# Optimization experiments

Measured on AMD Instinct MI355X. Metric: run time of the kernel, lower is better.

The kernel has to match this reference:

```python
import jax, jax.numpy as jnp
import numpy as np

N = 100000   # nodes
E = 1600000  # edges
D = 64       # feature dim (input = hidden = output)
G = 256      # graphs in batch
EPS = 1e-5   # BatchNorm eps


def setup_inputs() -> dict:
    key = jax.random.key(0)
    ks = jax.random.split(key, 16)
    inp = {
        "x": jax.random.normal(ks[0], (N, D), dtype=jnp.float32),
        "edge_index": jax.random.randint(ks[1], (2, E), 0, N, dtype=jnp.int64),
        "batch": jnp.sort(jax.random.randint(ks[2], (N,), 0, G, dtype=jnp.int64)),
    }
    # GCNConv weights (glorot-ish) + biases, and BatchNorm affine params, 3 layers
    for i in range(3):
        inp[f"W{i+1}"] = jax.random.normal(ks[3 + i], (D, D), dtype=jnp.float32) / np.sqrt(D)
        inp[f"b{i+1}"] = jnp.zeros((D,), dtype=jnp.float32)
        inp[f"g{i+1}"] = jnp.ones((D,), dtype=jnp.float32)   # BN gamma
        inp[f"be{i+1}"] = jnp.zeros((D,), dtype=jnp.float32)  # BN beta
    return inp


def _batchnorm(x, gamma, beta):
    # BatchNorm1d in training mode: batch stats over the node dim (biased var)
    mean = jnp.mean(x, axis=0)
    var = jnp.mean(jnp.square(x - mean), axis=0)
    return (x - mean) * jax.lax.rsqrt(var + EPS) * gamma + beta


def reference(x, edge_index, batch, W1, b1, g1, be1, W2, b2, g2, be2, W3, b3, g3, be3):
    src, dst = edge_index[0], edge_index[1]
    # GCN normalization with self-loops: norm_ij = deg_i^-1/2 * deg_j^-1/2 over A + I
    loop = jnp.arange(N, dtype=src.dtype)
    src2 = jnp.concatenate([src, loop])
    dst2 = jnp.concatenate([dst, loop])
    deg = jax.ops.segment_sum(jnp.ones_like(src2, dtype=x.dtype), dst2, num_segments=N)
    dinv = jax.lax.rsqrt(deg)  # deg >= 1 thanks to self loops
    norm = (dinv[src2] * dinv[dst2])[:, None]  # [E+N, 1]

    def gcn_conv(h, W, b):
        h = h @ W                                   # [N, D] small GEMM
        msg = h[src2] * norm                        # per-edge gather (memory bound)
        return jax.ops.segment_sum(msg, dst2, num_segments=N) + b

    params = [(W1, b1, g1, be1), (W2, b2, g2, be2), (W3, b3, g3, be3)]
    h = x
    for i, (W, b, g, be) in enumerate(params):
        h = gcn_conv(h, W, b)
        h = _batchnorm(h, g, be)
        if i < 2:
            h = jax.nn.relu(h)
            # dropout(p=0.2) is identity in deterministic/eval reference

    # global mean + max pool per graph
    ones = jnp.ones((N,), dtype=h.dtype)
    cnt = jax.ops.segment_sum(ones, batch, num_segments=G)            # [G]
    s = jax.ops.segment_sum(h, batch, num_segments=G)                 # [G, D]
    mean = s / jnp.maximum(cnt, 1.0)[:, None]
    mx = jax.ops.segment_max(h, batch, num_segments=G)
    mx = jnp.where(cnt[:, None] > 0, mx, 0.0)
    return mean + mx
```

## Files before the change

### kernel.cpp

```cpp
#include <hip/hip_runtime.h>
#include <hip/hip_bf16.h>
#include <math.h>

#define N_NODES 100000
#define N_EDGES 1600000
#define DIM 64
#define N_GRAPHS 256
#define BN_EPS 1e-5f
#define N_XCD 8
#define BUCKET ((N_NODES + N_XCD - 1) / N_XCD)
#define FILL_CHUNKS 128
#define FILL_ESIZE ((N_EDGES + FILL_CHUNKS - 1) / FILL_CHUNKS)
#define CSR_STRIDE 48
#define HIST_BLOCKS (FILL_CHUNKS * N_XCD)
#define GEMM0_BLOCKS 1024

__device__ inline unsigned short f2bf(float f) {
    __hip_bfloat16 h = __float2bfloat16(f);
    return *reinterpret_cast<unsigned short*>(&h);
}
__device__ inline unsigned int pack2bf(float a, float b) {
    return (unsigned int)f2bf(a) | ((unsigned int)f2bf(b) << 16);
}
__device__ inline float bf_lo(unsigned int u) { return __uint_as_float(u << 16); }
__device__ inline float bf_hi(unsigned int u) { return __uint_as_float(u & 0xffff0000u); }

__global__ __launch_bounds__(256) void hist_gemm0(const int* __restrict__ src,
                                                  const int* __restrict__ dst,
                                                  int* __restrict__ cnt,
                                                  int* __restrict__ csr_pad,
                                                  const float* __restrict__ x,
                                                  const float* __restrict__ W,
                                                  unsigned short* __restrict__ tbA,
                                                  unsigned short* __restrict__ tbB) {
    if (blockIdx.x < HIST_BLOCKS) {
        int chunk = blockIdx.x >> 3;
        int lo = (blockIdx.x & (N_XCD - 1)) * BUCKET;
        int e0 = chunk * FILL_ESIZE;
        int e1 = min(e0 + FILL_ESIZE, N_EDGES);
        for (int e = e0 + threadIdx.x; e < e1; e += 256) {
            int d = __builtin_nontemporal_load(&dst[e]);
            if ((unsigned)(d - lo) < (unsigned)BUCKET) {
                int r = atomicAdd(&cnt[d], 1);
                csr_pad[d * CSR_STRIDE + r] = __builtin_nontemporal_load(&src[e]);
            }
        }
    } else {
        int tid = threadIdx.x;
        int d = tid & 63;
        int wv = tid >> 6;
        float wcol[64];
        #pragma unroll
        for (int k = 0; k < 64; ++k) wcol[k] = W[k * 64 + d];
        unsigned short* tdst = (d < 32) ? (tbA + d) : (tbB + (d - 32));
        int gb = blockIdx.x - HIST_BLOCKS;
        int nwaves = GEMM0_BLOCKS * 4;
        for (int row = gb * 4 + wv; row < N_NODES; row += nwaves) {
            int urow = __builtin_amdgcn_readfirstlane(row);
            const float* hr = x + (size_t)urow * 64;
            float a0 = 0.f, a1 = 0.f, a2 = 0.f, a3 = 0.f;
            #pragma unroll
            for (int k = 0; k < 64; k += 4) {
                a0 = fmaf(hr[k + 0], wcol[k + 0], a0);
                a1 = fmaf(hr[k + 1], wcol[k + 1], a1);
                a2 = fmaf(hr[k + 2], wcol[k + 2], a2);
                a3 = fmaf(hr[k + 3], wcol[k + 3], a3);
            }
            float acc = (a0 + a1) + (a2 + a3);
            tdst[(size_t)urow * 32] = f2bf(acc);
        }
    }
}

__global__ __launch_bounds__(256) void finish_scale(const int* __restrict__ cnt,
                                                    unsigned short* __restrict__ tbA,
                                                    unsigned short* __restrict__ tbB,
                                                    float* __restrict__ dinv) {
    const int per_arr = N_NODES * 4;
    for (int i = blockIdx.x * 256 + threadIdx.x; i < 2 * per_arr; i += gridDim.x * 256) {
        int second = (i >= per_arr);
        int j = second ? (i - per_arr) : i;
        int row = j >> 2;
        float di = rsqrtf((float)(cnt[row] + 1));
        unsigned short* p = (second ? tbB : tbA) + (size_t)j * 8;
        uint4 u = *reinterpret_cast<const uint4*>(p);
        uint4 o;
        o.x = pack2bf(bf_lo(u.x) * di, bf_hi(u.x) * di);
        o.y = pack2bf(bf_lo(u.y) * di, bf_hi(u.y) * di);
        o.z = pack2bf(bf_lo(u.z) * di, bf_hi(u.z) * di);
        o.w = pack2bf(bf_lo(u.w) * di, bf_hi(u.w) * di);
        *reinterpret_cast<uint4*>(p) = o;
        if (!second && (j & 3) == 0) dinv[row] = di;
    }
}

__global__ __launch_bounds__(256) void bn_gemm_v(const unsigned short* __restrict__ aggA,
                                                 const unsigned short* __restrict__ aggB,
                                                 const float* __restrict__ stats,
                                                 const float* __restrict__ gamma,
                                                 const float* __restrict__ beta,
                                                 const float* __restrict__ W,
                                                 const float* __restrict__ dinv,
                                                 unsigned short* __restrict__ tbA,
                                                 unsigned short* __restrict__ tbB) {
    __shared__ float abuf[4][64];
    __shared__ float scale_s[64], shift_s[64];
    int tid = threadIdx.x;
    int d = tid & 63;
    int wv = tid >> 6;
    if (tid < 64) {
        const float inv_n = 1.0f / (float)N_NODES;
        float mean = stats[tid] * inv_n;
        float var = fmaxf(stats[64 + tid] * inv_n - mean * mean, 0.f);
        float rs = rsqrtf(var + BN_EPS) * gamma[tid];
        scale_s[tid] = rs;
        shift_s[tid] = beta[tid] - mean * rs;
    }
    float wcol[64];
    #pragma unroll
    for (int k = 0; k < 64; ++k) wcol[k] = W[k * 64 + d];
    __syncthreads();
    float sc = scale_s[d], sh = shift_s[d];
    const unsigned short* hsrc = (d < 32) ? (aggA + d) : (aggB + (d - 32));
    unsigned short* tdst = (d < 32) ? (tbA + d) : (tbB + (d - 32));
    const float4* av = reinterpret_cast<const float4*>(abuf[wv]);
    int nwaves = gridDim.x * 4;
    int row = blockIdx.x * 4 + wv;
    unsigned short hraw = 0;
    if (row < N_NODES) hraw = hsrc[(size_t)row * 32];
    while (row < N_NODES) {
        int nrow = row + nwaves;
        unsigned short hnraw = 0;
        if (nrow < N_NODES) hnraw = hsrc[(size_t)nrow * 32];
        float di = dinv[row];
        float h = __uint_as_float(((unsigned int)hraw) << 16);
        float a = fmaxf(fmaf(h, sc, sh), 0.f);
        abuf[wv][d] = a;
        float a0 = 0.f, a1 = 0.f, a2 = 0.f, a3 = 0.f;
        #pragma unroll
        for (int k4 = 0; k4 < 16; ++k4) {
            float4 v = av[k4];
            int k = k4 * 4;
            a0 = fmaf(v.x, wcol[k + 0], a0);
            a1 = fmaf(v.y, wcol[k + 1], a1);
            a2 = fmaf(v.z, wcol[k + 2], a2);
            a3 = fmaf(v.w, wcol[k + 3], a3);
        }
        float acc = (a0 + a1) + (a2 + a3);
        tdst[(size_t)row * 32] = f2bf(acc * di);
        row = nrow;
        hraw = hnraw;
    }
}

__global__ __launch_bounds__(256) void gather_agg(const int* __restrict__ csr_pad,
                                                  const int* __restrict__ cnt,
                                                  const float* __restrict__ dinv,
                                                  const unsigned short* __restrict__ tbA,
                                                  const unsigned short* __restrict__ tbB,
                                                  const float* __restrict__ bias,
                                                  unsigned short* __restrict__ aggA,
                                                  unsigned short* __restrict__ aggB,
                                                  float* __restrict__ stats) {
    int tid = threadIdx.x;
    int wave = tid >> 6;
    int lane = tid & 63;
    int o    = lane >> 3;
    int c    = lane & 7;

    int g8   = blockIdx.x & 7;
    int half = (g8 >= 4) ? 1 : 0;
    int hbid = (blockIdx.x >> 3) * 4 + (g8 & 3);
    const unsigned short* tbH  = half ? tbB : tbA;
    unsigned short*       aggH = half ? aggB : aggA;
    const float*          biH  = bias + half * 32;

    float4 s4  = {0.f, 0.f, 0.f, 0.f};
    float4 sq4 = {0.f, 0.f, 0.f, 0.f};

    for (int v = hbid * 4 + wave; v < N_NODES; v += 4096) {
        int beg = v * CSR_STRIDE;
        int end = beg + cnt[v];
        float4 A = {0,0,0,0}, B = {0,0,0,0};
        int e = beg;
        for (; e + 16 <= end; e += 16) {
            int s0 = csr_pad[e + o];
            int s1 = csr_pad[e + 8 + o];
            uint2 u0 = *reinterpret_cast<const uint2*>(tbH + (size_t)s0 * 32 + c * 4);
            uint2 u1 = *reinterpret_cast<const uint2*>(tbH + (size_t)s1 * 32 + c * 4);
            A.x += bf_lo(u0.x); A.y += bf_hi(u0.x); A.z += bf_lo(u0.y); A.w += bf_hi(u0.y);
            B.x += bf_lo(u1.x); B.y += bf_hi(u1.x); B.z += bf_lo(u1.y); B.w += bf_hi(u1.y);
        }
        for (; e + o < end; e += 8) {
            int s0 = csr_pad[e + o];
            uint2 u0 = *reinterpret_cast<const uint2*>(tbH + (size_t)s0 * 32 + c * 4);
            A.x += bf_lo(u0.x); A.y += bf_hi(u0.x); A.z += bf_lo(u0.y); A.w += bf_hi(u0.y);
        }
        A.x += B.x; A.y += B.y; A.z += B.z; A.w += B.w;

        A.x += __shfl_xor(A.x, 8, 64); A.x += __shfl_xor(A.x, 16, 64); A.x += __shfl_xor(A.x, 32, 64);
        A.y += __shfl_xor(A.y, 8, 64); A.y += __shfl_xor(A.y, 16, 64); A.y += __shfl_xor(A.y, 32, 64);
        A.z += __shfl_xor(A.z, 8, 64); A.z += __shfl_xor(A.z, 16, 64); A.z += __shfl_xor(A.z, 32, 64);
        A.w += __shfl_xor(A.w, 8, 64); A.w += __shfl_xor(A.w, 16, 64); A.w += __shfl_xor(A.w, 32, 64);

        if (o == 0) {
            float di = dinv[v];
            uint2 uv = *reinterpret_cast<const uint2*>(tbH + (size_t)v * 32 + c * 4);
            float4 bi = *reinterpret_cast<const float4*>(biH + c * 4);
            float4 val;
            val.x = fmaf(di, A.x + bf_lo(uv.x), bi.x);
            val.y = fmaf(di, A.y + bf_hi(uv.x), bi.y);
            val.z = fmaf(di, A.z + bf_lo(uv.y), bi.z);
            val.w = fmaf(di, A.w + bf_hi(uv.y), bi.w);
            uint2 ov;
            ov.x = pack2bf(val.x, val.y);
            ov.y = pack2bf(val.z, val.w);
            *reinterpret_cast<uint2*>(aggH + (size_t)v * 32 + c * 4) = ov;
            s4.x += val.x; s4.y += val.y; s4.z += val.z; s4.w += val.w;
            sq4.x += val.x * val.x; sq4.y += val.y * val.y;
            sq4.z += val.z * val.z; sq4.w += val.w * val.w;
        }
    }

    __shared__ float shs[4][32];
    __shared__ float shq[4][32];
    if (o == 0) {
        *reinterpret_cast<float4*>(&shs[wave][c * 4]) = s4;
        *reinterpret_cast<float4*>(&shq[wave][c * 4]) = sq4;
    }
    __syncthreads();
    if (tid < 32) {
        float S = shs[0][tid] + shs[1][tid] + shs[2][tid] + shs[3][tid];
        float Q = shq[0][tid] + shq[1][tid] + shq[2][tid] + shq[3][tid];
        unsafeAtomicAdd(&stats[half * 32 + tid], S);
        unsafeAtomicAdd(&stats[64 + half * 32 + tid], Q);
    }
}

__global__ __launch_bounds__(256) void pool_partial(const unsigned short* __restrict__ aggA,
                                                    const unsigned short* __restrict__ aggB,
                                                    const int* __restrict__ batch,
                                                    const float* __restrict__ stats,
                                                    const float* __restrict__ gamma,
                                                    const float* __restrict__ beta,
                                                    float* __restrict__ pS,
                                                    float* __restrict__ pM) {
    int bid = blockIdx.x;
    int g = bid >> 2, p = bid & 3;
    __shared__ float scale[64], shift[64];
    __shared__ int bounds[2];
    int tid = threadIdx.x;
    if (tid < 64) {
        const float inv_n = 1.0f / (float)N_NODES;
        float mean = stats[tid] * inv_n;
        float var = fmaxf(stats[64 + tid] * inv_n - mean * mean, 0.f);
        float rs = rsqrtf(var + BN_EPS) * gamma[tid];
        scale[tid] = rs;
        shift[tid] = beta[tid] - mean * rs;
    }
    if (tid < 2) {
        int target = g + tid;
        int lo = 0, hi = N_NODES;
        while (lo < hi) {
            int mid = (lo + hi) >> 1;
            if (batch[mid] < target) lo = mid + 1; else hi = mid;
        }
        bounds[tid] = lo;
    }
    __syncthreads();
    int lo = bounds[0], hi = bounds[1];
    int d = tid & 63, g4 = tid >> 6;
    const unsigned short* hsrc = (d < 32) ? (aggA + d) : (aggB + (d - 32));
    float sc = scale[d], sh = shift[d];
    float s = 0.f, m = -3.402823466e38f;
    for (int row = lo + p * 4 + g4; row < hi; row += 16) {
        float v = __uint_as_float(((unsigned int)hsrc[(size_t)row * 32]) << 16);
        v = fmaf(v, sc, sh);
        s += v;
        m = fmaxf(m, v);
    }
    __shared__ float shs[8][64];
    shs[g4][d] = s;
    shs[4 + g4][d] = m;
    __syncthreads();
    if (tid < 64) {
        float S = shs[0][tid] + shs[1][tid] + shs[2][tid] + shs[3][tid];
        float M = fmaxf(fmaxf(shs[4][tid], shs[5][tid]), fmaxf(shs[6][tid], shs[7][tid]));
        pS[bid * 64 + tid] = S;
        pM[bid * 64 + tid] = M;
    }
}

__global__ __launch_bounds__(64) void pool_final(const int* __restrict__ batch,
                                                 const float* __restrict__ pS,
                                                 const float* __restrict__ pM,
                                                 float* __restrict__ out) {
    int g = blockIdx.x, d = threadIdx.x;
    __shared__ int bounds[2];
    if (d < 2) {
        int target = g + d;
        int lo = 0, hi = N_NODES;
        while (lo < hi) {
            int mid = (lo + hi) >> 1;
            if (batch[mid] < target) lo = mid + 1; else hi = mid;
        }
        bounds[d] = lo;
    }
    __syncthreads();
    int cnt = bounds[1] - bounds[0];
    int base = g * 4 * 64 + d;
    float S = (pS[base] + pS[base + 64]) + (pS[base + 128] + pS[base + 192]);
    float M = fmaxf(fmaxf(pM[base], pM[base + 64]), fmaxf(pM[base + 128], pM[base + 192]));
    float mean = S / fmaxf((float)cnt, 1.0f);
    out[g * 64 + d] = (cnt > 0) ? (mean + M) : 0.0f;
}

extern "C" void kernel_launch(void* const* d_in, const int* in_sizes, int n_in,
                              void* d_out, int out_size, void* d_ws, size_t ws_size,
                              hipStream_t stream) {
    const float* x     = (const float*)d_in[0];
    const int*   eidx  = (const int*)d_in[1];
    const int*   batch = (const int*)d_in[2];
    const float* W[3]  = {(const float*)d_in[3], (const float*)d_in[7],  (const float*)d_in[11]};
    const float* b[3]  = {(const float*)d_in[4], (const float*)d_in[8],  (const float*)d_in[12]};
    const float* gm[3] = {(const float*)d_in[5], (const float*)d_in[9],  (const float*)d_in[13]};
    const float* be[3] = {(const float*)d_in[6], (const float*)d_in[10], (const float*)d_in[14]};

    unsigned short* tbA   = (unsigned short*)d_ws;
    unsigned short* tbB   = tbA + (size_t)N_NODES * 32;
    unsigned short* aggA  = tbB + (size_t)N_NODES * 32;
    unsigned short* aggB  = aggA + (size_t)N_NODES * 32;
    float* dinv     = (float*)(aggB + (size_t)N_NODES * 32);
    float* stats    = dinv + N_NODES;
    int*   cnt      = (int*)(stats + 384);
    float* poolS    = (float*)(cnt + N_NODES);
    float* poolM    = poolS + 1024 * 64;
    int*   csr_pad  = (int*)(poolM + 1024 * 64);

    const int* srcp = eidx;
    const int* dstp = eidx + N_EDGES;

    hipMemsetAsync(stats, 0, (384 + N_NODES) * sizeof(float), stream);

    hist_gemm0<<<HIST_BLOCKS + GEMM0_BLOCKS, 256, 0, stream>>>(srcp, dstp, cnt, csr_pad,
                                                               x, W[0], tbA, tbB);
    finish_scale<<<1024, 256, 0, stream>>>(cnt, tbA, tbB, dinv);

    gather_agg<<<2048, 256, 0, stream>>>(csr_pad, cnt, dinv, tbA, tbB, b[0], aggA, aggB, stats);

    bn_gemm_v<<<1024, 256, 0, stream>>>(aggA, aggB, stats, gm[0], be[0], W[1], dinv, tbA, tbB);
    gather_agg<<<2048, 256, 0, stream>>>(csr_pad, cnt, dinv, tbA, tbB, b[1], aggA, aggB, stats + 128);

    bn_gemm_v<<<1024, 256, 0, stream>>>(aggA, aggB, stats + 128, gm[1], be[1], W[2], dinv, tbA, tbB);
    gather_agg<<<2048, 256, 0, stream>>>(csr_pad, cnt, dinv, tbA, tbB, b[2], aggA, aggB, stats + 256);

    pool_partial<<<N_GRAPHS * 4, 256, 0, stream>>>(aggA, aggB, batch, stats + 256, gm[2], be[2], poolS, poolM);
    pool_final<<<N_GRAPHS, 64, 0, stream>>>(batch, poolS, poolM, (float*)d_out);
}
```

Baseline: 425.7 us.

## Split bf16 feature tables into four 16-column quarters for gather locality

Measured after the change: 558.8 us. +31.2%, slower.

```diff
diff --git a/kernel.cpp b/kernel.cpp
--- a/kernel.cpp
+++ b/kernel.cpp
@@ -14,6 +14,7 @@
 #define CSR_STRIDE 48
 #define HIST_BLOCKS (FILL_CHUNKS * N_XCD)
 #define GEMM0_BLOCKS 1024
+#define QS ((size_t)N_NODES * 16)
 
 __device__ inline unsigned short f2bf(float f) {
     __hip_bfloat16 h = __float2bfloat16(f);
@@ -31,8 +32,7 @@
                                                   int* __restrict__ csr_pad,
                                                   const float* __restrict__ x,
                                                   const float* __restrict__ W,
-                                                  unsigned short* __restrict__ tbA,
-                                                  unsigned short* __restrict__ tbB) {
+                                                  unsigned short* __restrict__ tbq) {
     if (blockIdx.x < HIST_BLOCKS) {
         int chunk = blockIdx.x >> 3;
         int lo = (blockIdx.x & (N_XCD - 1)) * BUCKET;
@@ -52,7 +52,7 @@
         float wcol[64];
         #pragma unroll
         for (int k = 0; k < 64; ++k) wcol[k] = W[k * 64 + d];
-        unsigned short* tdst = (d < 32) ? (tbA + d) : (tbB + (d - 32));
+        unsigned short* tdst = tbq + (size_t)(d >> 4) * QS + (d & 15);
         int gb = blockIdx.x - HIST_BLOCKS;
         int nwaves = GEMM0_BLOCKS * 4;
         for (int row = gb * 4 + wv; row < N_NODES; row += nwaves) {
@@ -67,42 +67,40 @@
                 a3 = fmaf(hr[k + 3], wcol[k + 3], a3);
             }
             float acc = (a0 + a1) + (a2 + a3);
-            tdst[(size_t)urow * 32] = f2bf(acc);
+            tdst[(size_t)urow * 16] = f2bf(acc);
         }
     }
 }
 
 __global__ __launch_bounds__(256) void finish_scale(const int* __restrict__ cnt,
-                                                    unsigned short* __restrict__ tbA,
-                                                    unsigned short* __restrict__ tbB,
+                                                    unsigned short* __restrict__ tbq,
                                                     float* __restrict__ dinv) {
-    const int per_arr = N_NODES * 4;
-    for (int i = blockIdx.x * 256 + threadIdx.x; i < 2 * per_arr; i += gridDim.x * 256) {
-        int second = (i >= per_arr);
-        int j = second ? (i - per_arr) : i;
-        int row = j >> 2;
+    const int total = N_NODES * 2;
+    for (int j = blockIdx.x * 256 + threadIdx.x; j < total; j += gridDim.x * 256) {
+        int row = j >> 1;
         float di = rsqrtf((float)(cnt[row] + 1));
-        unsigned short* p = (second ? tbB : tbA) + (size_t)j * 8;
-        uint4 u = *reinterpret_cast<const uint4*>(p);
-        uint4 o;
-        o.x = pack2bf(bf_lo(u.x) * di, bf_hi(u.x) * di);
-        o.y = pack2bf(bf_lo(u.y) * di, bf_hi(u.y) * di);
-        o.z = pack2bf(bf_lo(u.z) * di, bf_hi(u.z) * di);
-        o.w = pack2bf(bf_lo(u.w) * di, bf_hi(u.w) * di);
-        *reinterpret_cast<uint4*>(p) = o;
-        if (!second && (j & 3) == 0) dinv[row] = di;
-    }
-}
-
-__global__ __launch_bounds__(256) void bn_gemm_v(const unsigned short* __restrict__ aggA,
-                                                 const unsigned short* __restrict__ aggB,
+        #pragma unroll
+        for (int q = 0; q < 4; ++q) {
+            unsigned short* p = tbq + (size_t)q * QS + (size_t)j * 8;
+            uint4 u = *reinterpret_cast<const uint4*>(p);
+            uint4 o;
+            o.x = pack2bf(bf_lo(u.x) * di, bf_hi(u.x) * di);
+            o.y = pack2bf(bf_lo(u.y) * di, bf_hi(u.y) * di);
+            o.z = pack2bf(bf_lo(u.z) * di, bf_hi(u.z) * di);
+            o.w = pack2bf(bf_lo(u.w) * di, bf_hi(u.w) * di);
+            *reinterpret_cast<uint4*>(p) = o;
+        }
+        if ((j & 1) == 0) dinv[row] = di;
+    }
+}
+
+__global__ __launch_bounds__(256) void bn_gemm_v(const unsigned short* __restrict__ aggq,
                                                  const float* __restrict__ stats,
                                                  const float* __restrict__ gamma,
                                                  const float* __restrict__ beta,
                                                  const float* __restrict__ W,
                                                  const float* __restrict__ dinv,
-                                                 unsigned short* __restrict__ tbA,
-                                                 unsigned short* __restrict__ tbB) {
+                                                 unsigned short* __restrict__ tbq) {
     __shared__ float abuf[4][64];
     __shared__ float scale_s[64], shift_s[64];
     int tid = threadIdx.x;
@@ -121,17 +119,17 @@
     for (int k = 0; k < 64; ++k) wcol[k] = W[k * 64 + d];
     __syncthreads();
     float sc = scale_s[d], sh = shift_s[d];
-    const unsigned short* hsrc = (d < 32) ? (aggA + d) : (aggB + (d - 32));
-    unsigned short* tdst = (d < 32) ? (tbA + d) : (tbB + (d - 32));
+    const unsigned short* hsrc = aggq + (size_t)(d >> 4) * QS + (d & 15);
+    unsigned short* tdst = tbq + (size_t)(d >> 4) * QS + (d & 15);
     const float4* av = reinterpret_cast<const float4*>(abuf[wv]);
     int nwaves = gridDim.x * 4;
     int row = blockIdx.x * 4 + wv;
     unsigned short hraw = 0;
-    if (row < N_NODES) hraw = hsrc[(size_t)row * 32];
+    if (row < N_NODES) hraw = hsrc[(size_t)row * 16];
     while (row < N_NODES) {
         int nrow = row + nwaves;
         unsigned short hnraw = 0;
-        if (nrow < N_NODES) hnraw = hsrc[(size_t)nrow * 32];
+        if (nrow < N_NODES) hnraw = hsrc[(size_t)nrow * 16];
         float di = dinv[row];
         float h = __uint_as_float(((unsigned int)hraw) << 16);
         float a = fmaxf(fmaf(h, sc, sh), 0.f);
@@ -147,7 +145,7 @@
             a3 = fmaf(v.w, wcol[k + 3], a3);
         }
         float acc = (a0 + a1) + (a2 + a3);
-        tdst[(size_t)row * 32] = f2bf(acc * di);
+        tdst[(size_t)row * 16] = f2bf(acc * di);
         row = nrow;
         hraw = hnraw;
     }
@@ -156,56 +154,58 @@
 __global__ __launch_bounds__(256) void gather_agg(const int* __restrict__ csr_pad,
                                                   const int* __restrict__ cnt,
                                                   const float* __restrict__ dinv,
-                                                  const unsigned short* __restrict__ tbA,
-                                                  const unsigned short* __restrict__ tbB,
+                                                  const unsigned short* __restrict__ tbq,
                                                   const float* __restrict__ bias,
-                                                  unsigned short* __restrict__ aggA,
-                                                  unsigned short* __restrict__ aggB,
+                                                  unsigned short* __restrict__ aggq,
                                                   float* __restrict__ stats) {
     int tid = threadIdx.x;
     int wave = tid >> 6;
     int lane = tid & 63;
-    int o    = lane >> 3;
-    int c    = lane & 7;
-
-    int g8   = blockIdx.x & 7;
-    int half = (g8 >= 4) ? 1 : 0;
-    int hbid = (blockIdx.x >> 3) * 4 + (g8 & 3);
-    const unsigned short* tbH  = half ? tbB : tbA;
-    unsigned short*       aggH = half ? aggB : aggA;
-    const float*          biH  = bias + half * 32;
+    int o    = lane >> 2;
+    int c    = lane & 3;
+
+    int g8  = blockIdx.x & 7;
+    int q   = g8 >> 1;
+    int sub = g8 & 1;
+    int hbid = blockIdx.x >> 3;
+    const unsigned short* tbH = tbq + (size_t)q * QS;
+    unsigned short*      aggH = aggq + (size_t)q * QS;
+    const float*          biH = bias + q * 16;
 
     float4 s4  = {0.f, 0.f, 0.f, 0.f};
     float4 sq4 = {0.f, 0.f, 0.f, 0.f};
 
-    for (int v = hbid * 4 + wave; v < N_NODES; v += 4096) {
+    for (int v = ((hbid << 1) | sub) * 4 + wave; v < N_NODES; v += 2048) {
         int beg = v * CSR_STRIDE;
         int end = beg + cnt[v];
-        float4 A = {0,0,0,0}, B = {0,0,0,0};
+        float4 A = {0.f, 0.f, 0.f, 0.f};
         int e = beg;
         for (; e + 16 <= end; e += 16) {
-            int s0 = csr_pad[e + o];
-            int s1 = csr_pad[e + 8 + o];
-            uint2 u0 = *reinterpret_cast<const uint2*>(tbH + (size_t)s0 * 32 + c * 4);
-            uint2 u1 = *reinterpret_cast<const uint2*>(tbH + (size_t)s1 * 32 + c * 4);
-            A.x += bf_lo(u0.x); A.y += bf_hi(u0.x); A.z += bf_lo(u0.y); A.w += bf_hi(u0.y);
-            B.x += bf_lo(u1.x); B.y += bf_hi(u1.x); B.z += bf_lo(u1.y); B.w += bf_hi(u1.y);
-        }
-        for (; e + o < end; e += 8) {
-            int s0 = csr_pad[e + o];
-            uint2 u0 = *reinterpret_cast<const uint2*>(tbH + (size_t)s0 * 32 + c * 4);
-            A.x += bf_lo(u0.x); A.y += bf_hi(u0.x); A.z += bf_lo(u0.y); A.w += bf_hi(u0.y);
-        }
-        A.x += B.x; A.y += B.y; A.z += B.z; A.w += B.w;
-
-        A.x += __shfl_xor(A.x, 8, 64); A.x += __shfl_xor(A.x, 16, 64); A.x += __shfl_xor(A.x, 32, 64);
-        A.y += __shfl_xor(A.y, 8, 64); A.y += __shfl_xor(A.y, 16, 64); A.y += __shfl_xor(A.y, 32, 64);
-        A.z += __shfl_xor(A.z, 8, 64); A.z += __shfl_xor(A.z, 16, 64); A.z += __shfl_xor(A.z, 32, 64);
-        A.w += __shfl_xor(A.w, 8, 64); A.w += __shfl_xor(A.w, 16, 64); A.w += __shfl_xor(A.w, 32, 64);
+            int s0 = __builtin_nontemporal_load(&csr_pad[e + o]);
+            uint2 u0 = *reinterpret_cast<const uint2*>(tbH + (size_t)s0 * 16 + c * 4);
+            A.x += bf_lo(u0.x); A.y += bf_hi(u0.x);
+            A.z += bf_lo(u0.y); A.w += bf_hi(u0.y);
+        }
+        int rem = end - e;
+        if (o < rem) {
+            int s0 = __builtin_nontemporal_load(&csr_pad[e + o]);
+            uint2 u0 = *reinterpret_cast<const uint2*>(tbH + (size_t)s0 * 16 + c * 4);
+            A.x += bf_lo(u0.x); A.y += bf_hi(u0.x);
+            A.z += bf_lo(u0.y); A.w += bf_hi(u0.y);
+        }
+
+        A.x += __shfl_xor(A.x, 4, 64); A.x += __shfl_xor(A.x, 8, 64);
+        A.x += __shfl_xor(A.x, 16, 64); A.x += __shfl_xor(A.x, 32, 64);
+        A.y += __shfl_xor(A.y, 4, 64); A.y += __shfl_xor(A.y, 8, 64);
+        A.y += __shfl_xor(A.y, 16, 64); A.y += __shfl_xor(A.y, 32, 64);
+        A.z += __shfl_xor(A.z, 4, 64); A.z += __shfl_xor(A.z, 8, 64);
+        A.z += __shfl_xor(A.z, 16, 64); A.z += __shfl_xor(A.z, 32, 64);
+        A.w += __shfl_xor(A.w, 4, 64); A.w += __shfl_xor(A.w, 8, 64);
+        A.w += __shfl_xor(A.w, 16, 64); A.w += __shfl_xor(A.w, 32, 64);
 
         if (o == 0) {
             float di = dinv[v];
-            uint2 uv = *reinterpret_cast<const uint2*>(tbH + (size_t)v * 32 + c * 4);
+            uint2 uv = *reinterpret_cast<const uint2*>(tbH + (size_t)v * 16 + c * 4);
             float4 bi = *reinterpret_cast<const float4*>(biH + c * 4);
             float4 val;
             val.x = fmaf(di, A.x + bf_lo(uv.x), bi.x);
@@ -215,30 +215,29 @@
             uint2 ov;
             ov.x = pack2bf(val.x, val.y);
             ov.y = pack2bf(val.z, val.w);
-            *reinterpret_cast<uint2*>(aggH + (size_t)v * 32 + c * 4) = ov;
+            *reinterpret_cast<uint2*>(aggH + (size_t)v * 16 + c * 4) = ov;
             s4.x += val.x; s4.y += val.y; s4.z += val.z; s4.w += val.w;
             sq4.x += val.x * val.x; sq4.y += val.y * val.y;
             sq4.z += val.z * val.z; sq4.w += val.w * val.w;
         }
     }
 
-    __shared__ float shs[4][32];
-    __shared__ float shq[4][32];
+    __shared__ float shs[4][16];
+    __shared__ float shq[4][16];
     if (o == 0) {
         *reinterpret_cast<float4*>(&shs[wave][c * 4]) = s4;
         *reinterpret_cast<float4*>(&shq[wave][c * 4]) = sq4;
     }
     __syncthreads();
-    if (tid < 32) {
+    if (tid < 16) {
         float S = shs[0][tid] + shs[1][tid] + shs[2][tid] + shs[3][tid];
         float Q = shq[0][tid] + shq[1][tid] + shq[2][tid] + shq[3][tid];
-        unsafeAtomicAdd(&stats[half * 32 + tid], S);
-        unsafeAtomicAdd(&stats[64 + half * 32 + tid], Q);
-    }
-}
-
-__global__ __launch_bounds__(256) void pool_partial(const unsigned short* __restrict__ aggA,
-                                                    const unsigned short* __restrict__ aggB,
+        unsafeAtomicAdd(&stats[q * 16 + tid], S);
+        unsafeAtomicAdd(&stats[64 + q * 16 + tid], Q);
+    }
+}
+
+__global__ __launch_bounds__(256) void pool_partial(const unsigned short* __restrict__ aggq,
                                                     const int* __restrict__ batch,
                                                     const float* __restrict__ stats,
                                                     const float* __restrict__ gamma,
@@ -270,11 +269,11 @@
     __syncthreads();
     int lo = bounds[0], hi = bounds[1];
     int d = tid & 63, g4 = tid >> 6;
-    const unsigned short* hsrc = (d < 32) ? (aggA + d) : (aggB + (d - 32));
+    const unsigned short* hsrc = aggq + (size_t)(d >> 4) * QS + (d & 15);
     float sc = scale[d], sh = shift[d];
     float s = 0.f, m = -3.402823466e38f;
     for (int row = lo + p * 4 + g4; row < hi; row += 16) {
-        float v = __uint_as_float(((unsigned int)hsrc[(size_t)row * 32]) << 16);
+        float v = __uint_as_float(((unsigned int)hsrc[(size_t)row * 16]) << 16);
         v = fmaf(v, sc, sh);
         s += v;
         m = fmaxf(m, v);
@@ -326,11 +325,9 @@
     const float* gm[3] = {(const float*)d_in[5], (const float*)d_in[9],  (const float*)d_in[13]};
     const float* be[3] = {(const float*)d_in[6], (const float*)d_in[10], (const float*)d_in[14]};
 
-    unsigned short* tbA   = (unsigned short*)d_ws;
-    unsigned short* tbB   = tbA + (size_t)N_NODES * 32;
-    unsigned short* aggA  = tbB + (size_t)N_NODES * 32;
-    unsigned short* aggB  = aggA + (size_t)N_NODES * 32;
-    float* dinv     = (float*)(aggB + (size_t)N_NODES * 32);
+    unsigned short* tbq   = (unsigned short*)d_ws;
+    unsigned short* aggq  = tbq + 4 * QS;
+    float* dinv     = (float*)(aggq + 4 * QS);
     float* stats    = dinv + N_NODES;
     int*   cnt      = (int*)(stats + 384);
     float* poolS    = (float*)(cnt + N_NODES);
@@ -343,17 +340,17 @@
     hipMemsetAsync(stats, 0, (384 + N_NODES) * sizeof(float), stream);
 
     hist_gemm0<<<HIST_BLOCKS + GEMM0_BLOCKS, 256, 0, stream>>>(srcp, dstp, cnt, csr_pad,
-                                                               x, W[0], tbA, tbB);
-    finish_scale<<<1024, 256, 0, stream>>>(cnt, tbA, tbB, dinv);
-
-    gather_agg<<<2048, 256, 0, stream>>>(csr_pad, cnt, dinv, tbA, tbB, b[0], aggA, aggB, stats);
-
-    bn_gemm_v<<<1024, 256, 0, stream>>>(aggA, aggB, stats, gm[0], be[0], W[1], dinv, tbA, tbB);
-    gather_agg<<<2048, 256, 0, stream>>>(csr_pad, cnt, dinv, tbA, tbB, b[1], aggA, aggB, stats + 128);
-
-    bn_gemm_v<<<1024, 256, 0, stream>>>(aggA, aggB, stats + 128, gm[1], be[1], W[2], dinv, tbA, tbB);
-    gather_agg<<<2048, 256, 0, stream>>>(csr_pad, cnt, dinv, tbA, tbB, b[2], aggA, aggB, stats + 256);
-
-    pool_partial<<<N_GRAPHS * 4, 256, 0, stream>>>(aggA, aggB, batch, stats + 256, gm[2], be[2], poolS, poolM);
+                                                               x, W[0], tbq);
+    finish_scale<<<1024, 256, 0, stream>>>(cnt, tbq, dinv);
+
+    gather_agg<<<2048, 256, 0, stream>>>(csr_pad, cnt, dinv, tbq, b[0], aggq, stats);
+
+    bn_gemm_v<<<1024, 256, 0, stream>>>(aggq, stats, gm[0], be[0], W[1], dinv, tbq);
+    gather_agg<<<2048, 256, 0, stream>>>(csr_pad, cnt, dinv, tbq, b[1], aggq, stats + 128);
+
+    bn_gemm_v<<<1024, 256, 0, stream>>>(aggq, stats + 128, gm[1], be[1], W[2], dinv, tbq);
+    gather_agg<<<2048, 256, 0, stream>>>(csr_pad, cnt, dinv, tbq, b[2], aggq, stats + 256);
+
+    pool_partial<<<N_GRAPHS * 4, 256, 0, stream>>>(aggq, batch, stats + 256, gm[2], be[2], poolS, poolM);
     pool_final<<<N_GRAPHS, 64, 0, stream>>>(batch, poolS, poolM, (float*)d_out);
 }
```
